# Performance work log

Hardware: AMD Instinct MI355X
Metric: run time of the kernel (lower is better)

The kernel has to match this reference:

```python
import jax, jax.numpy as jnp
import numpy as np

SIZE = 11
SIGMA = 1.5
PAD = 5

def _window2d():
    # cv2.getGaussianKernel(11, 1.5): normalized 1D Gaussian, outer product -> 2D window
    x = np.arange(SIZE) - (SIZE - 1) / 2.0
    g = np.exp(-(x * x) / (2.0 * SIGMA * SIGMA))
    g = g / g.sum()
    return jnp.asarray(np.outer(g, g), dtype=jnp.float32)

def _gconv(x, w):
    # x: [H, W]; replicate ('edge') pad by 5 then valid 11x11 correlation (matches torch
    # Conv2d with padding_mode='replicate'); output [H, W]
    xp = jnp.pad(x, PAD, mode='edge')[None, None]  # [1,1,H+10,W+10]
    y = jax.lax.conv_general_dilated(
        xp, w[None, None], window_strides=(1, 1), padding='VALID',
        dimension_numbers=('NCHW', 'OIHW', 'NCHW'))
    return y[0, 0]

def setup_inputs() -> dict:
    key = jax.random.key(0)
    k1, k2 = jax.random.split(key)
    H = W = 4096
    img1 = jax.random.uniform(k1, (H, W), dtype=jnp.float32) * 255.0
    img2 = jax.random.uniform(k2, (H, W), dtype=jnp.float32) * 255.0
    return {"img1": img1, "img2": img2}

def reference(img1, img2):
    w = _window2d()
    C1 = (0.01 * 255) ** 2
    C2 = (0.03 * 255) ** 2
    mu1 = _gconv(img1, w)
    mu2 = _gconv(img2, w)
    mu1_sq = mu1 * mu1
    mu2_sq = mu2 * mu2
    mu1_mu2 = mu1 * mu2
    sigma1_sq = _gconv(img1 * img1, w) - mu1_sq
    sigma2_sq = _gconv(img2 * img2, w) - mu2_sq
    sigma12 = _gconv(img1 * img2, w) - mu1_mu2
    ssim_map = (2 * mu1_mu2 + C1) * (2 * sigma12 + C2) / (
        (mu1_sq + mu2_sq + C1) * (sigma1_sq + sigma2_sq + C2))
    return jnp.mean(ssim_map)
```

## Files before the change

kernel.cpp:

```cpp
#include <hip/hip_runtime.h>
#include <cmath>

#define IMG_H 4096
#define IMG_W 4096
#define GX 8
#define GY 64
#define TCOLS 512
#define WCOLS 128
#define R 64
#define NITER (R + 10)
#define SW 144
#define RWORDS (2*SW)
#define NBUF 3

struct GW { float w[11]; };

__device__ __forceinline__ int clampi(int v, int lo, int hi) {
  return v < lo ? lo : (v > hi ? hi : v);
}

__global__ __launch_bounds__(256, 2) void ssim_sweep_kernel(
    const float* __restrict__ img1, const float* __restrict__ img2,
    float* __restrict__ partial, GW gw) {
  __shared__ __align__(16) float sbuf[4][NBUF][RWORDS];

  const int tid  = threadIdx.x;
  const int wv   = tid >> 6;
  const int lane = tid & 63;
  const int bx = blockIdx.x, by = blockIdx.y;
  const int cw   = bx * TCOLS + wv * WCOLS;
  const int row0 = by * R;
  const bool ledge = (cw == 0), redge = (cw + WCOLS == IMG_W);

  const int   jjA   = (lane < 36) ? lane : lane - 36;
  const float* baseA = (lane < 36) ? img1 : img2;
  const int   coA   = clampi(cw - 8 + 4 * jjA, 0, IMG_W - 4);
  const int   coB   = clampi(cw - 8 + 4 * (lane + 28), 0, IMG_W - 4);

  float* swv = &sbuf[wv][0][0];

  auto stage = [&](int slot, int i) {
    const int gr = clampi(row0 - 5 + i, 0, IMG_H - 1);
    const long rb = (long)gr * IMG_W;
    float* dst = swv + slot * RWORDS;
    __builtin_amdgcn_global_load_lds(
        (const __attribute__((address_space(1))) void*)(baseA + rb + coA),
        (__attribute__((address_space(3))) void*)dst, 16, 0, 0);
    if (lane < 8) {
      __builtin_amdgcn_global_load_lds(
          (const __attribute__((address_space(1))) void*)(img2 + rb + coB),
          (__attribute__((address_space(3))) void*)(dst + 256), 16, 0, 0);
    }
  };

  stage(0, 0);
  stage(1, 1);

  float A[4][11][2];
  float sum = 0.f;
  const float C1 = 6.5025f, C2 = 58.5225f;
  const int base = 2 * lane + 2;

  int cur = 0;

  #pragma unroll 1
  for (int i = 0; i < NITER; ++i) {
    const int pre = (cur == 0) ? 2 : cur - 1;
    stage(pre, i + 2);

    asm volatile("s_waitcnt vmcnt(4)" ::: "memory");
    __builtin_amdgcn_sched_barrier(0);

    float* buf = swv + cur * RWORDS;
    cur = (cur == 2) ? 0 : cur + 1;

    if (ledge || redge) {
      if (lane < 16) {
        const int im = lane >> 3, l = lane & 7;
        const int srcw = im * SW + (ledge ? 8 : 135);
        const int dstw = im * SW + (ledge ? l : 136 + l);
        buf[dstw] = buf[srcw];
      }
    }

    float wa[14], wb[14];
    #pragma unroll
    for (int m = 0; m < 7; ++m) {
      float2 fa = *reinterpret_cast<const float2*>(&buf[base + 2 * m]);
      float2 fb = *reinterpret_cast<const float2*>(&buf[SW + base + 2 * m]);
      wa[2 * m] = fa.x; wa[2 * m + 1] = fa.y;
      wb[2 * m] = fb.x; wb[2 * m + 1] = fb.y;
    }

    float h[4][2];
    #pragma unroll
    for (int ch = 0; ch < 4; ++ch) { h[ch][0] = 0.f; h[ch][1] = 0.f; }
    #pragma unroll
    for (int e = 1; e <= 12; ++e) {
      const float a = wa[e], b = wb[e];
      const float sq = fmaf(b, b, a * a);
      const float ab = a * b;
      if (e <= 11) {
        const float w0 = gw.w[e - 1];
        h[0][0] = fmaf(w0, a,  h[0][0]);
        h[1][0] = fmaf(w0, b,  h[1][0]);
        h[2][0] = fmaf(w0, sq, h[2][0]);
        h[3][0] = fmaf(w0, ab, h[3][0]);
      }
      if (e >= 2) {
        const float w1 = gw.w[e - 2];
        h[0][1] = fmaf(w1, a,  h[0][1]);
        h[1][1] = fmaf(w1, b,  h[1][1]);
        h[2][1] = fmaf(w1, sq, h[2][1]);
        h[3][1] = fmaf(w1, ab, h[3][1]);
      }
    }

    #pragma unroll
    for (int ch = 0; ch < 4; ++ch) {
      #pragma unroll
      for (int x = 0; x < 2; ++x) {
        const float hv = h[ch][x];
        #pragma unroll
        for (int k = 0; k < 10; ++k)
          A[ch][k][x] = fmaf(gw.w[10 - k], hv, A[ch][k + 1][x]);
        A[ch][10][x] = gw.w[0] * hv;
      }
    }

    if (i >= 10) {
      #pragma unroll
      for (int x = 0; x < 2; ++x) {
        float mu1 = A[0][0][x], mu2 = A[1][0][x];
        float s3  = A[2][0][x], s4  = A[3][0][x];
        float mu1s = mu1 * mu1, mu2s = mu2 * mu2, m12 = mu1 * mu2;
        float num = (2.f * m12 + C1) * (2.f * (s4 - m12) + C2);
        float den = (mu1s + mu2s + C1) * ((s3 - mu1s - mu2s) + C2);
        sum += num * __builtin_amdgcn_rcpf(den);
      }
    }
  }

  #pragma unroll
  for (int off = 32; off > 0; off >>= 1) sum += __shfl_down(sum, off);
  __shared__ float wsum[4];
  if (lane == 0) wsum[wv] = sum;
  __syncthreads();
  if (tid == 0)
    partial[by * GX + bx] = wsum[0] + wsum[1] + wsum[2] + wsum[3];
}

__global__ __launch_bounds__(256) void ssim_reduce_kernel(
    const float* __restrict__ partial, float* __restrict__ out) {
  int tid = threadIdx.x;
  double s = (double)partial[tid] + (double)partial[tid + 256];
  #pragma unroll
  for (int off = 32; off > 0; off >>= 1) s += __shfl_down(s, off);
  __shared__ double ws[4];
  if ((tid & 63) == 0) ws[tid >> 6] = s;
  __syncthreads();
  if (tid == 0)
    out[0] = (float)((ws[0] + ws[1] + ws[2] + ws[3]) /
                     ((double)IMG_H * (double)IMG_W));
}

extern "C" void kernel_launch(void* const* d_in, const int* in_sizes, int n_in,
                              void* d_out, int out_size, void* d_ws, size_t ws_size,
                              hipStream_t stream) {
  const float* img1 = (const float*)d_in[0];
  const float* img2 = (const float*)d_in[1];
  float* partial = (float*)d_ws;
  float* out = (float*)d_out;

  GW gw;
  double g[11], s = 0.0;
  for (int i = 0; i < 11; ++i) {
    double x = i - 5.0;
    g[i] = exp(-(x * x) / (2.0 * 1.5 * 1.5));
    s += g[i];
  }
  for (int i = 0; i < 11; ++i) gw.w[i] = (float)(g[i] / s);

  dim3 grid(GX, GY);
  ssim_sweep_kernel<<<grid, 256, 0, stream>>>(img1, img2, partial, gw);
  ssim_reduce_kernel<<<1, 256, 0, stream>>>(partial, out);
}
```

Measured before the change: 201.0 us.

## Switch to one output column per lane with narrower wave tiles

Each lane now computes one output column instead of two, so a wave covers 64 columns and the grid doubles along x. Per-lane register state (the vertical accumulator array and the horizontal window) halves, and launch bounds are raised to target three blocks per SIMD. In exchange, the horizontal halo overhead per loaded row grows relative to the useful columns, and the register reuse from sharing window loads between two adjacent outputs is lost. The staging, LDS layout, wait counts and final reduction are adjusted to match the new tile size.

```diff
diff --git a/kernel.cpp b/kernel.cpp
--- a/kernel.cpp
+++ b/kernel.cpp
@@ -3,13 +3,13 @@
 
 #define IMG_H 4096
 #define IMG_W 4096
-#define GX 8
+#define GX 16
 #define GY 64
-#define TCOLS 512
-#define WCOLS 128
+#define TCOLS 256
+#define WCOLS 64
 #define R 64
 #define NITER (R + 10)
-#define SW 144
+#define SW 80
 #define RWORDS (2*SW)
 #define NBUF 3
 
@@ -19,7 +19,7 @@
   return v < lo ? lo : (v > hi ? hi : v);
 }
 
-__global__ __launch_bounds__(256, 2) void ssim_sweep_kernel(
+__global__ __launch_bounds__(256, 3) void ssim_sweep_kernel(
     const float* __restrict__ img1, const float* __restrict__ img2,
     float* __restrict__ partial, GW gw) {
   __shared__ __align__(16) float sbuf[4][NBUF][RWORDS];
@@ -32,10 +32,9 @@
   const int row0 = by * R;
   const bool ledge = (cw == 0), redge = (cw + WCOLS == IMG_W);
 
-  const int   jjA   = (lane < 36) ? lane : lane - 36;
-  const float* baseA = (lane < 36) ? img1 : img2;
-  const int   coA   = clampi(cw - 8 + 4 * jjA, 0, IMG_W - 4);
-  const int   coB   = clampi(cw - 8 + 4 * (lane + 28), 0, IMG_W - 4);
+  const float* srcp = (lane < 20) ? img1 : img2;
+  const int    co   = clampi(cw - 8 + 4 * ((lane < 20) ? lane : lane - 20),
+                             0, IMG_W - 4);
 
   float* swv = &sbuf[wv][0][0];
 
@@ -43,23 +42,20 @@
     const int gr = clampi(row0 - 5 + i, 0, IMG_H - 1);
     const long rb = (long)gr * IMG_W;
     float* dst = swv + slot * RWORDS;
-    __builtin_amdgcn_global_load_lds(
-        (const __attribute__((address_space(1))) void*)(baseA + rb + coA),
-        (__attribute__((address_space(3))) void*)dst, 16, 0, 0);
-    if (lane < 8) {
+    if (lane < 40) {
       __builtin_amdgcn_global_load_lds(
-          (const __attribute__((address_space(1))) void*)(img2 + rb + coB),
-          (__attribute__((address_space(3))) void*)(dst + 256), 16, 0, 0);
+          (const __attribute__((address_space(1))) void*)(srcp + rb + co),
+          (__attribute__((address_space(3))) void*)dst, 16, 0, 0);
     }
   };
 
   stage(0, 0);
   stage(1, 1);
 
-  float A[4][11][2];
+  float A[4][11];
   float sum = 0.f;
   const float C1 = 6.5025f, C2 = 58.5225f;
-  const int base = 2 * lane + 2;
+  const int wl = lane + 3;
 
   int cur = 0;
 
@@ -68,7 +64,7 @@
     const int pre = (cur == 0) ? 2 : cur - 1;
     stage(pre, i + 2);
 
-    asm volatile("s_waitcnt vmcnt(4)" ::: "memory");
+    asm volatile("s_waitcnt vmcnt(2)" ::: "memory");
     __builtin_amdgcn_sched_barrier(0);
 
     float* buf = swv + cur * RWORDS;
@@ -77,67 +73,45 @@
     if (ledge || redge) {
       if (lane < 16) {
         const int im = lane >> 3, l = lane & 7;
-        const int srcw = im * SW + (ledge ? 8 : 135);
-        const int dstw = im * SW + (ledge ? l : 136 + l);
+        const int srcw = im * SW + (ledge ? 8 : 71);
+        const int dstw = im * SW + (ledge ? l : 72 + l);
         buf[dstw] = buf[srcw];
       }
     }
 
-    float wa[14], wb[14];
+    float h0 = 0.f, h1 = 0.f, h2 = 0.f, h3 = 0.f;
     #pragma unroll
-    for (int m = 0; m < 7; ++m) {
-      float2 fa = *reinterpret_cast<const float2*>(&buf[base + 2 * m]);
-      float2 fb = *reinterpret_cast<const float2*>(&buf[SW + base + 2 * m]);
-      wa[2 * m] = fa.x; wa[2 * m + 1] = fa.y;
-      wb[2 * m] = fb.x; wb[2 * m + 1] = fb.y;
-    }
-
-    float h[4][2];
-    #pragma unroll
-    for (int ch = 0; ch < 4; ++ch) { h[ch][0] = 0.f; h[ch][1] = 0.f; }
-    #pragma unroll
-    for (int e = 1; e <= 12; ++e) {
-      const float a = wa[e], b = wb[e];
+    for (int j = 0; j <= 10; ++j) {
+      const float a = buf[wl + j];
+      const float b = buf[SW + wl + j];
+      const float w = gw.w[j];
       const float sq = fmaf(b, b, a * a);
       const float ab = a * b;
-      if (e <= 11) {
-        const float w0 = gw.w[e - 1];
-        h[0][0] = fmaf(w0, a,  h[0][0]);
-        h[1][0] = fmaf(w0, b,  h[1][0]);
-        h[2][0] = fmaf(w0, sq, h[2][0]);
-        h[3][0] = fmaf(w0, ab, h[3][0]);
-      }
-      if (e >= 2) {
-        const float w1 = gw.w[e - 2];
-        h[0][1] = fmaf(w1, a,  h[0][1]);
-        h[1][1] = fmaf(w1, b,  h[1][1]);
-        h[2][1] = fmaf(w1, sq, h[2][1]);
-        h[3][1] = fmaf(w1, ab, h[3][1]);
-      }
+      h0 = fmaf(w, a,  h0);
+      h1 = fmaf(w, b,  h1);
+      h2 = fmaf(w, sq, h2);
+      h3 = fmaf(w, ab, h3);
     }
 
     #pragma unroll
-    for (int ch = 0; ch < 4; ++ch) {
-      #pragma unroll
-      for (int x = 0; x < 2; ++x) {
-        const float hv = h[ch][x];
-        #pragma unroll
-        for (int k = 0; k < 10; ++k)
-          A[ch][k][x] = fmaf(gw.w[10 - k], hv, A[ch][k + 1][x]);
-        A[ch][10][x] = gw.w[0] * hv;
-      }
+    for (int k = 0; k < 10; ++k) {
+      A[0][k] = fmaf(gw.w[10 - k], h0, A[0][k + 1]);
+      A[1][k] = fmaf(gw.w[10 - k], h1, A[1][k + 1]);
+      A[2][k] = fmaf(gw.w[10 - k], h2, A[2][k + 1]);
+      A[3][k] = fmaf(gw.w[10 - k], h3, A[3][k + 1]);
     }
+    A[0][10] = gw.w[0] * h0;
+    A[1][10] = gw.w[0] * h1;
+    A[2][10] = gw.w[0] * h2;
+    A[3][10] = gw.w[0] * h3;
 
     if (i >= 10) {
-      #pragma unroll
-      for (int x = 0; x < 2; ++x) {
-        float mu1 = A[0][0][x], mu2 = A[1][0][x];
-        float s3  = A[2][0][x], s4  = A[3][0][x];
-        float mu1s = mu1 * mu1, mu2s = mu2 * mu2, m12 = mu1 * mu2;
-        float num = (2.f * m12 + C1) * (2.f * (s4 - m12) + C2);
-        float den = (mu1s + mu2s + C1) * ((s3 - mu1s - mu2s) + C2);
-        sum += num * __builtin_amdgcn_rcpf(den);
-      }
+      const float mu1 = A[0][0], mu2 = A[1][0];
+      const float s3  = A[2][0], s4  = A[3][0];
+      const float mu1s = mu1 * mu1, mu2s = mu2 * mu2, m12 = mu1 * mu2;
+      const float num = (2.f * m12 + C1) * (2.f * (s4 - m12) + C2);
+      const float den = (mu1s + mu2s + C1) * ((s3 - mu1s - mu2s) + C2);
+      sum += num * __builtin_amdgcn_rcpf(den);
     }
   }
 
@@ -153,7 +127,8 @@
 __global__ __launch_bounds__(256) void ssim_reduce_kernel(
     const float* __restrict__ partial, float* __restrict__ out) {
   int tid = threadIdx.x;
-  double s = (double)partial[tid] + (double)partial[tid + 256];
+  double s = (double)partial[tid] + (double)partial[tid + 256] +
+             (double)partial[tid + 512] + (double)partial[tid + 768];
   #pragma unroll
   for (int off = 32; off > 0; off >>= 1) s += __shfl_down(s, off);
   __shared__ double ws[4];
```

Measured after the change: 187.5 us. 1.07x faster.
